# Kernel tuning notes

Measured on AMD Instinct MI355X. Metric: run time of the kernel, lower is better.

## Reference

```python
import jax, jax.numpy as jnp
import numpy as np

BATCH, SEQ, IN_DIM, HID = 256, 256, 128, 512
KMAX, MID, NCLS = 4, 256, 16  # maxout features, maxout/dense/highway width, output classes


def hard_sigmoid(x):
    return jnp.clip(0.2 * x + 0.5, 0.0, 1.0)


def setup_inputs() -> dict:
    key = jax.random.key(0)
    ks = jax.random.split(key, 20)
    s = 0.05
    d = {
        'x': jax.random.normal(ks[0], (BATCH, SEQ, IN_DIM), jnp.float32),
        'W_z': jax.random.normal(ks[1], (IN_DIM, HID), jnp.float32) * s,
        'W_r': jax.random.normal(ks[2], (IN_DIM, HID), jnp.float32) * s,
        'W_h': jax.random.normal(ks[3], (IN_DIM, HID), jnp.float32) * s,
        'U_z': jax.random.normal(ks[4], (HID, HID), jnp.float32) * s,
        'U_r': jax.random.normal(ks[5], (HID, HID), jnp.float32) * s,
        'U_h': jax.random.normal(ks[6], (HID, HID), jnp.float32) * s,
        'b_z': jax.random.normal(ks[7], (HID,), jnp.float32) * s,
        'b_r': jax.random.normal(ks[8], (HID,), jnp.float32) * s,
        'b_h': jax.random.normal(ks[9], (HID,), jnp.float32) * s,
        'mo_W': jax.random.normal(ks[10], (KMAX, HID, MID), jnp.float32) * s,
        'mo_b': jax.random.normal(ks[11], (KMAX, MID), jnp.float32) * s,
        'd1_W': jax.random.normal(ks[12], (MID, MID), jnp.float32) * s,
        'd1_b': jax.random.normal(ks[13], (MID,), jnp.float32) * s,
        'hw_W': jax.random.normal(ks[14], (MID, MID), jnp.float32) * s,
        'hw_b': jax.random.normal(ks[15], (MID,), jnp.float32) * s,
        'hw_Wc': jax.random.normal(ks[16], (MID, MID), jnp.float32) * s,
        'hw_bc': jax.random.normal(ks[17], (MID,), jnp.float32) * s,
        'd2_W': jax.random.normal(ks[18], (MID, NCLS), jnp.float32) * s,
        'd2_b': jax.random.normal(ks[19], (NCLS,), jnp.float32) * s,
    }
    return d


def reference(x, W_z, W_r, W_h, U_z, U_r, U_h, b_z, b_r, b_h,
              mo_W, mo_b, d1_W, d1_b, hw_W, hw_b, hw_Wc, hw_bc, d2_W, d2_b):
    # ---- Theano-convention GRU (reset applied before U_h matmul) ----
    # Precompute all input projections in one batched GEMM each: [B,S,H]
    xz = jnp.einsum('bsi,ih->bsh', x, W_z) + b_z
    xr = jnp.einsum('bsi,ih->bsh', x, W_r) + b_r
    xh = jnp.einsum('bsi,ih->bsh', x, W_h) + b_h

    def step(h, xs):
        xzt, xrt, xht = xs
        z = hard_sigmoid(xzt + h @ U_z)
        r = hard_sigmoid(xrt + h @ U_r)
        hh = jnp.tanh(xht + (r * h) @ U_h)
        h_new = z * h + (1.0 - z) * hh
        return h_new, None

    h0 = jnp.zeros((x.shape[0], U_z.shape[0]), x.dtype)
    # scan over time axis: move S to leading dim
    xs = (jnp.swapaxes(xz, 0, 1), jnp.swapaxes(xr, 0, 1), jnp.swapaxes(xh, 0, 1))
    h, _ = jax.lax.scan(step, h0, xs)

    # ---- Maxout dense ----
    h = jnp.max(jnp.einsum('bi,kio->bko', h, mo_W) + mo_b, axis=1)
    # ---- Dense (linear) ----
    h = h @ d1_W + d1_b
    # ---- Highway ----
    t = jax.nn.sigmoid(h @ hw_Wc + hw_bc)
    hh = jax.nn.relu(h @ hw_W + hw_b)
    h = t * hh + (1.0 - t) * h
    # ---- Dense + softmax ----
    logits = h @ d2_W + d2_b
    return jax.nn.softmax(logits, axis=-1)
```

## Files before the change

### kernel.cpp

```cpp
#include <hip/hip_runtime.h>
#include <hip/hip_bf16.h>
#include <math.h>

#define BATCH 256
#define SEQN  256
#define INDIM 128
#define HID   512
#define MID   256
#define NCLS  16

#define NG 8
#define RG 32
#define NS 16
#define SC 32

typedef _Float16 half8 __attribute__((ext_vector_type(8)));
typedef float    f32x4 __attribute__((ext_vector_type(4)));

__device__ __forceinline__ half8 cc_load16(const _Float16* p) {
    half8 r;
    asm volatile("global_load_dwordx4 %0, %1, off sc1" : "=&v"(r) : "v"(p));
    return r;
}
__device__ __forceinline__ void cc_wait() {
    asm volatile("s_waitcnt vmcnt(0)" ::: "memory");
    __builtin_amdgcn_sched_barrier(0);
}
__device__ __forceinline__ void cc_store16(_Float16* p, _Float16 v) {
    unsigned short u = __builtin_bit_cast(unsigned short, v);
    asm volatile("global_store_short %0, %1, off sc1" :: "v"(p), "v"(u) : "memory");
}
__device__ __forceinline__ void cc_store_u32(unsigned int* p, unsigned int v) {
    asm volatile("global_store_dword %0, %1, off sc1" :: "v"(p), "v"(v) : "memory");
}
__device__ __forceinline__ unsigned int cc_load_u32(const unsigned int* p) {
    unsigned int r;
    asm volatile("global_load_dword %0, %1, off sc1\n\ts_waitcnt vmcnt(0)"
                 : "=&v"(r) : "v"(p) : "memory");
    return r;
}

__device__ __forceinline__ void group_barrier(unsigned int* base, int s, int l,
                                              unsigned int tgt) {
    if (l == 0) cc_store_u32(base + s, tgt);
    unsigned int v;
    do {
        v = cc_load_u32(base + (l & 15));
    } while (!__all((int)(v >= tgt)));
}

__global__ __launch_bounds__(256) void pack_wA(
    const float* __restrict__ Uz, const float* __restrict__ Ur,
    const float* __restrict__ Wz, const float* __restrict__ Wr,
    _Float16* __restrict__ out)
{
    int idx = blockIdx.x * 256 + threadIdx.x;
    int j = idx & 7, l = (idx >> 3) & 63;
    int fr = idx >> 9;
    int kt = fr % 20; int r2 = fr / 20;
    int nt4 = r2 & 3; int s = r2 >> 2;
    int k = kt * 32 + (l >> 4) * 8 + j;
    int col = s * SC + (nt4 & 1) * 16 + (l & 15);
    const float* U = (nt4 < 2) ? Uz : Ur;
    const float* W = (nt4 < 2) ? Wz : Wr;
    float v = (k < HID) ? U[k * HID + col] : W[(k - HID) * HID + col];
    out[idx] = (_Float16)v;
}

__global__ __launch_bounds__(256) void pack_wB(
    const float* __restrict__ Uh, const float* __restrict__ Wh,
    _Float16* __restrict__ out)
{
    int idx = blockIdx.x * 256 + threadIdx.x;
    int j = idx & 7, l = (idx >> 3) & 63;
    int fr = idx >> 9;
    int kt = fr % 20; int r2 = fr / 20;
    int nt2 = r2 & 1; int s = r2 >> 1;
    int k = kt * 32 + (l >> 4) * 8 + j;
    int col = s * SC + nt2 * 16 + (l & 15);
    float v = (k < HID) ? Uh[k * HID + col] : Wh[(k - HID) * HID + col];
    out[idx] = (_Float16)v;
}

__global__ __launch_bounds__(512) void gru_sync(
    const float* __restrict__ x, const _Float16* __restrict__ GWA,
    const _Float16* __restrict__ GWB,
    const float* __restrict__ bz, const float* __restrict__ br,
    const float* __restrict__ bh,
    _Float16* __restrict__ HF, _Float16* __restrict__ VF,
    unsigned int* __restrict__ arr, float* __restrict__ hout)
{
    __shared__ __attribute__((aligned(16))) _Float16 WA[4][20][64][8];
    __shared__ __attribute__((aligned(16))) _Float16 WB[2][20][64][8];
    __shared__ __attribute__((aligned(16))) _Float16 XB[2][16][64][8];
    __shared__ float HO[RG][SC];

    const int tid = threadIdx.x;
    const int w = tid >> 6, l = tid & 63;
    const int bid = blockIdx.x;
    const int g = bid & 7, s = bid >> 3;
    const int m = l & 15;
    const int crow0 = (l >> 4) * 4;

    const int mt  = w & 1;
    const int nt4 = w >> 1;
    const int nt2 = w >> 1;

    {
        const float4* srcA = (const float4*)&GWA[(size_t)s * (4 * 20 * 512)];
        float4* dstA = (float4*)&WA[0][0][0][0];
        for (int i = tid; i < 4 * 20 * 512 / 8; i += 512) dstA[i] = srcA[i];
        const float4* srcB = (const float4*)&GWB[(size_t)s * (2 * 20 * 512)];
        float4* dstB = (float4*)&WB[0][0][0][0];
        for (int i = tid; i < 2 * 20 * 512 / 8; i += 512) dstB[i] = srcB[i];
    }
    for (int i = tid; i < RG * SC; i += 512) ((float*)HO)[i] = 0.f;

    float biasA;
    {
        int col = s * SC + (nt4 & 1) * 16 + m;
        biasA = (nt4 < 2) ? bz[col] : br[col];
    }
    float biasB = 0.f;
    if (w < 4) biasB = bh[s * SC + nt2 * 16 + m];

    unsigned int* abase = &arr[g * 64];
    __syncthreads();

    float zreg[4];
    half8 xfr[4];

    for (int t = 0; t < SEQN; ++t) {
        {
            const _Float16* src = &HF[(size_t)g * (2 * 16 * 512)];
            half8 tmp0 = cc_load16(src + (tid +    0) * 8);
            half8 tmp1 = cc_load16(src + (tid +  512) * 8);
            half8 tmp2 = cc_load16(src + (tid + 1024) * 8);
            half8 tmp3 = cc_load16(src + (tid + 1536) * 8);

            const float* xp = &x[(((size_t)(g * RG + mt * 16 + m)) * SEQN + t) * INDIM + (l >> 4) * 8];
            float4 xa[4], xb[4];
            #pragma unroll
            for (int kf = 0; kf < 4; ++kf) {
                xa[kf] = *(const float4*)(xp + kf * 32);
                xb[kf] = *(const float4*)(xp + kf * 32 + 4);
            }
            cc_wait();
            half8* dst = (half8*)&XB[0][0][0][0];
            dst[tid +    0] = tmp0;
            dst[tid +  512] = tmp1;
            dst[tid + 1024] = tmp2;
            dst[tid + 1536] = tmp3;

            #pragma unroll
            for (int kf = 0; kf < 4; ++kf) {
                half8 hx;
                hx[0] = (_Float16)xa[kf].x; hx[1] = (_Float16)xa[kf].y;
                hx[2] = (_Float16)xa[kf].z; hx[3] = (_Float16)xa[kf].w;
                hx[4] = (_Float16)xb[kf].x; hx[5] = (_Float16)xb[kf].y;
                hx[6] = (_Float16)xb[kf].z; hx[7] = (_Float16)xb[kf].w;
                xfr[kf] = hx;
            }
        }
        __syncthreads();

        {
            f32x4 acc = {0.f, 0.f, 0.f, 0.f};
            #pragma unroll
            for (int kt = 0; kt < 16; ++kt) {
                half8 af = *(const half8*)&XB[mt][kt][l][0];
                half8 bf = *(const half8*)&WA[nt4][kt][l][0];
                acc = __builtin_amdgcn_mfma_f32_16x16x32_f16(af, bf, acc, 0, 0, 0);
            }
            #pragma unroll
            for (int kf = 0; kf < 4; ++kf) {
                half8 bf = *(const half8*)&WA[nt4][16 + kf][l][0];
                acc = __builtin_amdgcn_mfma_f32_16x16x32_f16(xfr[kf], bf, acc, 0, 0, 0);
            }
            if (nt4 < 2) {
                #pragma unroll
                for (int ri = 0; ri < 4; ++ri) {
                    float pre = acc[ri] + biasA;
                    zreg[ri] = fminf(fmaxf(0.2f * pre + 0.5f, 0.f), 1.f);
                }
            } else {
                #pragma unroll
                for (int ri = 0; ri < 4; ++ri) {
                    float pre = acc[ri] + biasA;
                    float gr = fminf(fmaxf(0.2f * pre + 0.5f, 0.f), 1.f);
                    int rloc = mt * 16 + crow0 + ri;
                    int cs = (nt4 & 1) * 16 + m;
                    float vv = gr * HO[rloc][cs];
                    cc_store16(&VF[(((size_t)(g * 2 + mt) * 16 + s) * 64 +
                                    ((crow0 + ri) + 16 * (cs >> 3))) * 8 + (cs & 7)],
                               (_Float16)vv);
                }
            }
        }

        __syncthreads();
        if (w == 0) group_barrier(abase, s, l, (unsigned int)(2 * t + 1));
        __syncthreads();

        {
            const _Float16* src = &VF[(size_t)g * (2 * 16 * 512)];
            half8 tmp0 = cc_load16(src + (tid +    0) * 8);
            half8 tmp1 = cc_load16(src + (tid +  512) * 8);
            half8 tmp2 = cc_load16(src + (tid + 1024) * 8);
            half8 tmp3 = cc_load16(src + (tid + 1536) * 8);
            cc_wait();
            half8* dst = (half8*)&XB[0][0][0][0];
            dst[tid +    0] = tmp0;
            dst[tid +  512] = tmp1;
            dst[tid + 1024] = tmp2;
            dst[tid + 1536] = tmp3;
        }
        __syncthreads();

        if (w < 4) {
            f32x4 acc2 = {0.f, 0.f, 0.f, 0.f};
            #pragma unroll
            for (int kt = 0; kt < 16; ++kt) {
                half8 af = *(const half8*)&XB[mt][kt][l][0];
                half8 bf = *(const half8*)&WB[nt2][kt][l][0];
                acc2 = __builtin_amdgcn_mfma_f32_16x16x32_f16(af, bf, acc2, 0, 0, 0);
            }
            #pragma unroll
            for (int kf = 0; kf < 4; ++kf) {
                half8 bf = *(const half8*)&WB[nt2][16 + kf][l][0];
                acc2 = __builtin_amdgcn_mfma_f32_16x16x32_f16(xfr[kf], bf, acc2, 0, 0, 0);
            }
            #pragma unroll
            for (int ri = 0; ri < 4; ++ri) {
                float pre = acc2[ri] + biasB;
                float e  = __expf(2.f * pre);
                float hh = 1.f - 2.f / (e + 1.f);
                int rloc = mt * 16 + crow0 + ri;
                int cs = nt2 * 16 + m;
                float zz = zreg[ri];
                float ho = HO[rloc][cs];
                float hn = zz * ho + (1.f - zz) * hh;
                HO[rloc][cs] = hn;
                cc_store16(&HF[(((size_t)(g * 2 + mt) * 16 + s) * 64 +
                                ((crow0 + ri) + 16 * (cs >> 3))) * 8 + (cs & 7)],
                           (_Float16)hn);
            }
        }

        __syncthreads();
        if (w == 0) group_barrier(abase, s, l, (unsigned int)(2 * t + 2));
        __syncthreads();
    }

    for (int i = tid; i < RG * SC; i += 512) {
        int r = i >> 5, c = i & 31;
        hout[(size_t)(g * RG + r) * HID + s * SC + c] = HO[r][c];
    }
}

__global__ __launch_bounds__(256) void maxout_k(
    const float* __restrict__ h, const float* __restrict__ moW,
    const float* __restrict__ mob, float* __restrict__ m)
{
    const int ot = blockIdx.x, bt = blockIdx.y;
    __shared__ float sA[32][33];
    __shared__ float sB[4][32][33];
    const int tid = threadIdx.x;
    const int tx = tid & 15, ty = tid >> 4;
    const int b0 = bt * 32, o0 = ot * 32;
    const int lr = tid >> 3, lk4 = (tid & 7) << 2;

    float acc[4][2][2];
    #pragma unroll
    for (int p = 0; p < 4; ++p)
        acc[p][0][0] = acc[p][0][1] = acc[p][1][0] = acc[p][1][1] = 0.f;

    for (int kt = 0; kt < 16; ++kt) {
        const int k0 = kt * 32;
        float4 a = *reinterpret_cast<const float4*>(&h[(b0 + lr) * HID + k0 + lk4]);
        float4 wv[4];
        #pragma unroll
        for (int p = 0; p < 4; ++p)
            wv[p] = *reinterpret_cast<const float4*>(&moW[((size_t)p * HID + k0 + lr) * MID + o0 + lk4]);
        __syncthreads();
        sA[lk4+0][lr] = a.x; sA[lk4+1][lr] = a.y; sA[lk4+2][lr] = a.z; sA[lk4+3][lr] = a.w;
        #pragma unroll
        for (int p = 0; p < 4; ++p) {
            sB[p][lr][lk4+0] = wv[p].x; sB[p][lr][lk4+1] = wv[p].y;
            sB[p][lr][lk4+2] = wv[p].z; sB[p][lr][lk4+3] = wv[p].w;
        }
        __syncthreads();
        #pragma unroll
        for (int kk = 0; kk < 32; ++kk) {
            float a0 = sA[kk][ty*2], a1 = sA[kk][ty*2+1];
            #pragma unroll
            for (int p = 0; p < 4; ++p) {
                float w0 = sB[p][kk][tx*2], w1 = sB[p][kk][tx*2+1];
                acc[p][0][0] += a0*w0; acc[p][0][1] += a0*w1;
                acc[p][1][0] += a1*w0; acc[p][1][1] += a1*w1;
            }
        }
    }

    #pragma unroll
    for (int q = 0; q < 2; ++q)
        #pragma unroll
        for (int c = 0; c < 2; ++c) {
            const int row = b0 + ty*2 + q, col = o0 + tx*2 + c;
            float best = -1e30f;
            #pragma unroll
            for (int p = 0; p < 4; ++p)
                best = fmaxf(best, acc[p][q][c] + mob[p * MID + col]);
            m[row * MID + col] = best;
        }
}

__global__ __launch_bounds__(256) void dense1_k(
    const float* __restrict__ m, const float* __restrict__ W,
    const float* __restrict__ b, float* __restrict__ a1)
{
    const int jt = blockIdx.x, bt = blockIdx.y;
    __shared__ float sA[32][33];
    __shared__ float sB[32][33];
    const int tid = threadIdx.x;
    const int tx = tid & 15, ty = tid >> 4;
    const int b0 = bt * 32, j0 = jt * 32;
    const int lr = tid >> 3, lk4 = (tid & 7) << 2;

    float acc[2][2] = {{0.f,0.f},{0.f,0.f}};

    for (int kt = 0; kt < 8; ++kt) {
        const int k0 = kt * 32;
        float4 a  = *reinterpret_cast<const float4*>(&m[(b0 + lr) * MID + k0 + lk4]);
        float4 bv = *reinterpret_cast<const float4*>(&W[(k0 + lr) * MID + j0 + lk4]);
        __syncthreads();
        sA[lk4+0][lr] = a.x; sA[lk4+1][lr] = a.y; sA[lk4+2][lr] = a.z; sA[lk4+3][lr] = a.w;
        sB[lr][lk4+0] = bv.x; sB[lr][lk4+1] = bv.y; sB[lr][lk4+2] = bv.z; sB[lr][lk4+3] = bv.w;
        __syncthreads();
        #pragma unroll
        for (int kk = 0; kk < 32; ++kk) {
            float a0 = sA[kk][ty*2], a1v = sA[kk][ty*2+1];
            float w0 = sB[kk][tx*2], w1 = sB[kk][tx*2+1];
            acc[0][0] += a0*w0; acc[0][1] += a0*w1;
            acc[1][0] += a1v*w0; acc[1][1] += a1v*w1;
        }
    }

    #pragma unroll
    for (int q = 0; q < 2; ++q)
        #pragma unroll
        for (int c = 0; c < 2; ++c) {
            const int row = b0 + ty*2 + q, col = j0 + tx*2 + c;
            a1[row * MID + col] = acc[q][c] + b[col];
        }
}

__global__ __launch_bounds__(256) void highway_k(
    const float* __restrict__ a1,
    const float* __restrict__ hwW, const float* __restrict__ hwb,
    const float* __restrict__ hwWc, const float* __restrict__ hwbc,
    float* __restrict__ h2)
{
    const int jt = blockIdx.x, bt = blockIdx.y;
    __shared__ float sA[32][33];
    __shared__ float sBh[32][33];
    __shared__ float sBc[32][33];
    const int tid = threadIdx.x;
    const int tx = tid & 15, ty = tid >> 4;
    const int b0 = bt * 32, j0 = jt * 32;
    const int lr = tid >> 3, lk4 = (tid & 7) << 2;

    float acch[2][2] = {{0.f,0.f},{0.f,0.f}};
    float accc[2][2] = {{0.f,0.f},{0.f,0.f}};

    for (int kt = 0; kt < 8; ++kt) {
        const int k0 = kt * 32;
        float4 a   = *reinterpret_cast<const float4*>(&a1[(b0 + lr) * MID + k0 + lk4]);
        float4 bh4 = *reinterpret_cast<const float4*>(&hwW[(k0 + lr) * MID + j0 + lk4]);
        float4 bc4 = *reinterpret_cast<const float4*>(&hwWc[(k0 + lr) * MID + j0 + lk4]);
        __syncthreads();
        sA[lk4+0][lr] = a.x; sA[lk4+1][lr] = a.y; sA[lk4+2][lr] = a.z; sA[lk4+3][lr] = a.w;
        sBh[lr][lk4+0] = bh4.x; sBh[lr][lk4+1] = bh4.y; sBh[lr][lk4+2] = bh4.z; sBh[lr][lk4+3] = bh4.w;
        sBc[lr][lk4+0] = bc4.x; sBc[lr][lk4+1] = bc4.y; sBc[lr][lk4+2] = bc4.z; sBc[lr][lk4+3] = bc4.w;
        __syncthreads();
        #pragma unroll
        for (int kk = 0; kk < 32; ++kk) {
            float a0 = sA[kk][ty*2], a1v = sA[kk][ty*2+1];
            float h0 = sBh[kk][tx*2], h1 = sBh[kk][tx*2+1];
            float c0 = sBc[kk][tx*2], c1 = sBc[kk][tx*2+1];
            acch[0][0] += a0*h0; acch[0][1] += a0*h1;
            acch[1][0] += a1v*h0; acch[1][1] += a1v*h1;
            accc[0][0] += a0*c0; accc[0][1] += a0*c1;
            accc[1][0] += a1v*c0; accc[1][1] += a1v*c1;
        }
    }

    #pragma unroll
    for (int q = 0; q < 2; ++q)
        #pragma unroll
        for (int c = 0; c < 2; ++c) {
            const int row = b0 + ty*2 + q, col = j0 + tx*2 + c;
            float tt = 1.f / (1.f + expf(-(accc[q][c] + hwbc[col])));
            float hp = fmaxf(acch[q][c] + hwb[col], 0.f);
            float av = a1[row * MID + col];
            h2[row * MID + col] = tt * hp + (1.f - tt) * av;
        }
}

__global__ __launch_bounds__(256) void d2_softmax(
    const float* __restrict__ h2, const float* __restrict__ W,
    const float* __restrict__ b, float* __restrict__ out)
{
    const int b0 = blockIdx.x * 16;
    const int r = threadIdx.x >> 4, c = threadIdx.x & 15;
    const int row = b0 + r;

    float acc = b[c];
    for (int i = 0; i < MID; ++i)
        acc += h2[row * MID + i] * W[i * NCLS + c];

    float mx = acc;
    #pragma unroll
    for (int off = 8; off; off >>= 1)
        mx = fmaxf(mx, __shfl_xor(mx, off, 16));
    float e = expf(acc - mx);
    float sm = e;
    #pragma unroll
    for (int off = 8; off; off >>= 1)
        sm += __shfl_xor(sm, off, 16);
    out[row * NCLS + c] = e / sm;
}

extern "C" void kernel_launch(void* const* d_in, const int* in_sizes, int n_in,
                              void* d_out, int out_size, void* d_ws, size_t ws_size,
                              hipStream_t stream) {
    (void)in_sizes; (void)n_in; (void)out_size; (void)ws_size;

    const float* x    = (const float*)d_in[0];
    const float* Wz   = (const float*)d_in[1];
    const float* Wr   = (const float*)d_in[2];
    const float* Wh   = (const float*)d_in[3];
    const float* Uz   = (const float*)d_in[4];
    const float* Ur   = (const float*)d_in[5];
    const float* Uh   = (const float*)d_in[6];
    const float* bz   = (const float*)d_in[7];
    const float* br   = (const float*)d_in[8];
    const float* bh   = (const float*)d_in[9];
    const float* moW  = (const float*)d_in[10];
    const float* mob  = (const float*)d_in[11];
    const float* d1W  = (const float*)d_in[12];
    const float* d1b  = (const float*)d_in[13];
    const float* hwW  = (const float*)d_in[14];
    const float* hwb  = (const float*)d_in[15];
    const float* hwWc = (const float*)d_in[16];
    const float* hwbc = (const float*)d_in[17];
    const float* d2W  = (const float*)d_in[18];
    const float* d2b  = (const float*)d_in[19];
    float* out = (float*)d_out;

    char* ws = (char*)d_ws;
    _Float16* GWA = (_Float16*)(ws + 0);
    _Float16* GWB = (_Float16*)(ws + 1310720);
    _Float16* HF  = (_Float16*)(ws + 1966080);
    _Float16* VF  = (_Float16*)(ws + 2228224);
    unsigned int* arr = (unsigned int*)(ws + 2490368);
    float*    hbuf = (float*)(ws + 2492416);
    float*    mxb = (float*)(ws + 0);
    float*    a1b = (float*)(ws + 262144);
    float*    h2b = (float*)(ws + 524288);

    hipMemsetAsync(HF, 0, 262144, stream);
    hipMemsetAsync(arr, 0, 2048, stream);

    pack_wA<<<2560, 256, 0, stream>>>(Uz, Ur, Wz, Wr, GWA);
    pack_wB<<<1280, 256, 0, stream>>>(Uh, Wh, GWB);

    gru_sync<<<128, 512, 0, stream>>>(x, GWA, GWB, bz, br, bh, HF, VF, arr, hbuf);

    dim3 blk(256);
    maxout_k<<<dim3(8, 8), blk, 0, stream>>>(hbuf, moW, mob, mxb);
    dense1_k<<<dim3(8, 8), blk, 0, stream>>>(mxb, d1W, d1b, a1b);
    highway_k<<<dim3(8, 8), blk, 0, stream>>>(a1b, hwW, hwb, hwWc, hwbc, h2b);
    d2_softmax<<<16, blk, 0, stream>>>(h2b, d2W, d2b, out);
}
```

Baseline: 1.922 ms.

## Replace group barriers with per-phase flag waits and direct register loads

New measurement: 1.742 ms, median of 2. 1.1x faster.

```diff
diff --git a/kernel.cpp b/kernel.cpp
--- a/kernel.cpp
+++ b/kernel.cpp
@@ -40,13 +40,14 @@
     return r;
 }
 
-__device__ __forceinline__ void group_barrier(unsigned int* base, int s, int l,
-                                              unsigned int tgt) {
-    if (l == 0) cc_store_u32(base + s, tgt);
-    unsigned int v;
-    do {
-        v = cc_load_u32(base + (l & 15));
-    } while (!__all((int)(v >= tgt)));
+__device__ __forceinline__ void wait_flags(const unsigned int* base, int s,
+                                           int l, unsigned int tgt) {
+    const int slot = l & 15;
+    for (;;) {
+        unsigned int v = cc_load_u32(base + slot);
+        int ok = (slot == s) || (v >= tgt);
+        if (__all(ok)) break;
+    }
 }
 
 __global__ __launch_bounds__(256) void pack_wA(
@@ -92,7 +93,6 @@
 {
     __shared__ __attribute__((aligned(16))) _Float16 WA[4][20][64][8];
     __shared__ __attribute__((aligned(16))) _Float16 WB[2][20][64][8];
-    __shared__ __attribute__((aligned(16))) _Float16 XB[2][16][64][8];
     __shared__ float HO[RG][SC];
 
     const int tid = threadIdx.x;
@@ -124,53 +124,52 @@
     float biasB = 0.f;
     if (w < 4) biasB = bh[s * SC + nt2 * 16 + m];
 
-    unsigned int* abase = &arr[g * 64];
+    unsigned int* f1base = &arr[g * 16];
+    unsigned int* f2base = &arr[128 + g * 16];
+    unsigned int* f1own  = &arr[g * 16 + s];
+    unsigned int* f2own  = &arr[128 + g * 16 + s];
     __syncthreads();
 
     float zreg[4];
     half8 xfr[4];
 
     for (int t = 0; t < SEQN; ++t) {
+        float4 xa[4], xb[4];
         {
-            const _Float16* src = &HF[(size_t)g * (2 * 16 * 512)];
-            half8 tmp0 = cc_load16(src + (tid +    0) * 8);
-            half8 tmp1 = cc_load16(src + (tid +  512) * 8);
-            half8 tmp2 = cc_load16(src + (tid + 1024) * 8);
-            half8 tmp3 = cc_load16(src + (tid + 1536) * 8);
-
             const float* xp = &x[(((size_t)(g * RG + mt * 16 + m)) * SEQN + t) * INDIM + (l >> 4) * 8];
-            float4 xa[4], xb[4];
             #pragma unroll
             for (int kf = 0; kf < 4; ++kf) {
                 xa[kf] = *(const float4*)(xp + kf * 32);
                 xb[kf] = *(const float4*)(xp + kf * 32 + 4);
             }
-            cc_wait();
-            half8* dst = (half8*)&XB[0][0][0][0];
-            dst[tid +    0] = tmp0;
-            dst[tid +  512] = tmp1;
-            dst[tid + 1024] = tmp2;
-            dst[tid + 1536] = tmp3;
-
-            #pragma unroll
-            for (int kf = 0; kf < 4; ++kf) {
-                half8 hx;
-                hx[0] = (_Float16)xa[kf].x; hx[1] = (_Float16)xa[kf].y;
-                hx[2] = (_Float16)xa[kf].z; hx[3] = (_Float16)xa[kf].w;
-                hx[4] = (_Float16)xb[kf].x; hx[5] = (_Float16)xb[kf].y;
-                hx[6] = (_Float16)xb[kf].z; hx[7] = (_Float16)xb[kf].w;
-                xfr[kf] = hx;
-            }
-        }
-        __syncthreads();
+        }
+
+        wait_flags(f2base, s, l, (unsigned int)t);
+
+        half8 hfr[16];
+        {
+            const _Float16* hf = &HF[(size_t)(g * 2 + mt) * 16 * 512];
+            #pragma unroll
+            for (int kt = 0; kt < 16; ++kt)
+                hfr[kt] = cc_load16(hf + kt * 512 + l * 8);
+        }
+        #pragma unroll
+        for (int kf = 0; kf < 4; ++kf) {
+            half8 hx;
+            hx[0] = (_Float16)xa[kf].x; hx[1] = (_Float16)xa[kf].y;
+            hx[2] = (_Float16)xa[kf].z; hx[3] = (_Float16)xa[kf].w;
+            hx[4] = (_Float16)xb[kf].x; hx[5] = (_Float16)xb[kf].y;
+            hx[6] = (_Float16)xb[kf].z; hx[7] = (_Float16)xb[kf].w;
+            xfr[kf] = hx;
+        }
+        cc_wait();
 
         {
             f32x4 acc = {0.f, 0.f, 0.f, 0.f};
             #pragma unroll
             for (int kt = 0; kt < 16; ++kt) {
-                half8 af = *(const half8*)&XB[mt][kt][l][0];
                 half8 bf = *(const half8*)&WA[nt4][kt][l][0];
-                acc = __builtin_amdgcn_mfma_f32_16x16x32_f16(af, bf, acc, 0, 0, 0);
+                acc = __builtin_amdgcn_mfma_f32_16x16x32_f16(hfr[kt], bf, acc, 0, 0, 0);
             }
             #pragma unroll
             for (int kf = 0; kf < 4; ++kf) {
@@ -198,32 +197,27 @@
             }
         }
 
-        __syncthreads();
-        if (w == 0) group_barrier(abase, s, l, (unsigned int)(2 * t + 1));
-        __syncthreads();
-
-        {
-            const _Float16* src = &VF[(size_t)g * (2 * 16 * 512)];
-            half8 tmp0 = cc_load16(src + (tid +    0) * 8);
-            half8 tmp1 = cc_load16(src + (tid +  512) * 8);
-            half8 tmp2 = cc_load16(src + (tid + 1024) * 8);
-            half8 tmp3 = cc_load16(src + (tid + 1536) * 8);
+        asm volatile("s_waitcnt vmcnt(0)" ::: "memory");
+        __syncthreads();
+        if (tid == 0) cc_store_u32(f1own, (unsigned int)(t + 1));
+
+        if (w < 4) {
+            wait_flags(f1base, s, l, (unsigned int)(t + 1));
+
+            half8 vfr[16];
+            {
+                const _Float16* vf = &VF[(size_t)(g * 2 + mt) * 16 * 512];
+                #pragma unroll
+                for (int kt = 0; kt < 16; ++kt)
+                    vfr[kt] = cc_load16(vf + kt * 512 + l * 8);
+            }
             cc_wait();
-            half8* dst = (half8*)&XB[0][0][0][0];
-            dst[tid +    0] = tmp0;
-            dst[tid +  512] = tmp1;
-            dst[tid + 1024] = tmp2;
-            dst[tid + 1536] = tmp3;
-        }
-        __syncthreads();
-
-        if (w < 4) {
+
             f32x4 acc2 = {0.f, 0.f, 0.f, 0.f};
             #pragma unroll
             for (int kt = 0; kt < 16; ++kt) {
-                half8 af = *(const half8*)&XB[mt][kt][l][0];
                 half8 bf = *(const half8*)&WB[nt2][kt][l][0];
-                acc2 = __builtin_amdgcn_mfma_f32_16x16x32_f16(af, bf, acc2, 0, 0, 0);
+                acc2 = __builtin_amdgcn_mfma_f32_16x16x32_f16(vfr[kt], bf, acc2, 0, 0, 0);
             }
             #pragma unroll
             for (int kf = 0; kf < 4; ++kf) {
@@ -247,9 +241,9 @@
             }
         }
 
-        __syncthreads();
-        if (w == 0) group_barrier(abase, s, l, (unsigned int)(2 * t + 2));
-        __syncthreads();
+        asm volatile("s_waitcnt vmcnt(0)" ::: "memory");
+        __syncthreads();
+        if (tid == 0) cc_store_u32(f2own, (unsigned int)(t + 1));
     }
 
     for (int i = tid; i < RG * SC; i += 512) {
@@ -464,13 +458,13 @@
     _Float16* HF  = (_Float16*)(ws + 1966080);
     _Float16* VF  = (_Float16*)(ws + 2228224);
     unsigned int* arr = (unsigned int*)(ws + 2490368);
-    float*    hbuf = (float*)(ws + 2492416);
+    float*    hbuf = (float*)(ws + 2494464);
     float*    mxb = (float*)(ws + 0);
     float*    a1b = (float*)(ws + 262144);
     float*    h2b = (float*)(ws + 524288);
 
     hipMemsetAsync(HF, 0, 262144, stream);
-    hipMemsetAsync(arr, 0, 2048, stream);
+    hipMemsetAsync(arr, 0, 4096, stream);
 
     pack_wA<<<2560, 256, 0, stream>>>(Uz, Ur, Wz, Wr, GWA);
     pack_wB<<<1280, 256, 0, stream>>>(Uh, Wh, GWB);
```
